# Kernel optimization log

Hardware: AMD Instinct MI355X
Metric: run time of the kernel (lower is better)

The kernel has to match this reference:

```python
import jax, jax.numpy as jnp
import numpy as np

S, B, D, T, E, H = 8, 32, 5, 30, 768, 128


def _time_lstm(Wall, ball, Uall, bU, Wd, bd, x, ts):
    # x: [N,T,E], ts: [N,T]. Faithful to torch TimeLSTM: c_tmp uses sigmoid,
    # and the returned per-step 'outputs' are the o-gates (as in the source).
    N = x.shape[0]
    h0 = jnp.zeros((N, Wd.shape[0]), x.dtype)

    def step(carry, inp):
        h, c = carry
        xt, tt = inp
        c_s1 = jnp.tanh(c @ Wd + bd)
        c_adj = c - c_s1 + c_s1 * tt[:, None]
        g = jax.nn.sigmoid(h @ Wall + ball + xt @ Uall + bU)
        f, i, o, ct = jnp.split(g, 4, axis=1)
        c2 = f * c_adj + i * ct
        h2 = o * jnp.tanh(c2)
        return (h2, c2), o

    _, outs = jax.lax.scan(step, (h0, h0), (x.swapaxes(0, 1), ts.swapaxes(0, 1)))
    return outs.swapaxes(0, 1)  # [N,T,H]


def _attn(W1, b1, W2, b2, V, bV, full, last, lens):
    # full: [N,T,H]; last: [N,H] or [N,1,H]
    s1 = last @ W1 + b1
    if s1.ndim == 2:
        s1 = s1[:, None, :]
    score = jnp.tanh(s1 + full @ W2 + b2) @ V + bV  # [N,T,1]
    if lens is not None:
        mask = jnp.arange(full.shape[1])[None, :] < lens[:, None]
        score = jnp.where(mask[..., None], score, -jnp.inf)
    w = jax.nn.softmax(score, axis=1)
    return jnp.sum(w * full, axis=1)  # [N,H]


def _lstm(Wih, bih, Whh, bhh, x):
    # standard torch LSTM gate order i,f,g,o; x: [N,D,H]
    N = x.shape[0]
    Hh = Whh.shape[0]
    h0 = jnp.zeros((N, Hh), x.dtype)

    def step(carry, xt):
        h, c = carry
        g = xt @ Wih + bih + h @ Whh + bhh
        i, f, gg, o = jnp.split(g, 4, axis=1)
        c2 = jax.nn.sigmoid(f) * c + jax.nn.sigmoid(i) * jnp.tanh(gg)
        h2 = jax.nn.sigmoid(o) * jnp.tanh(c2)
        return (h2, c2), h2

    (h, c), hs = jax.lax.scan(step, (h0, h0), x.swapaxes(0, 1))
    return hs.swapaxes(0, 1), h  # [N,D,H], [N,H]


def _per_stock(tl_Wall, tl_ball, tl_Uall, tl_bU, tl_Wd, tl_bd,
               a1_W1, a1_b1, a1_W2, a1_b2, a1_V, a1_bV,
               l2_Wih, l2_bih, l2_Whh, l2_bhh,
               a2_W1, a2_b1, a2_W2, a2_b2, a2_V, a2_bV,
               x1_W, x1_b, x2_W, x2_b, sent, lens, times):
    # sent: [B,D,T,E], lens: [B,D] int, times: [B,D,T]
    b, d, t, e = sent.shape
    x = sent.reshape(b * d, t, e)
    ts = times.reshape(b * d, t)
    ln = lens.reshape(b * d)
    outs = _time_lstm(tl_Wall, tl_ball, tl_Uall, tl_bU, tl_Wd, tl_bd, x, ts)
    idx = jnp.clip(ln - 1, 0, t - 1)
    hn = outs[jnp.arange(b * d), idx]
    hn = jnp.where((ln > 0)[:, None], hn, 0.0)
    ctx = _attn(a1_W1, a1_b1, a1_W2, a1_b2, a1_V, a1_bV, outs, hn, ln)  # [B*D,H]
    seq = ctx.reshape(b, d, -1)
    hs, hlast = _lstm(l2_Wih, l2_bih, l2_Whh, l2_bhh, seq)
    ctx2 = _attn(a2_W1, a2_b1, a2_W2, a2_b2, a2_V, a2_bV, hs, hlast[:, None, :], None)
    y = jax.nn.relu(ctx2 @ x1_W + x1_b)  # dropout is eval-mode identity
    return y @ x2_W + x2_b  # [B,64]


def setup_inputs() -> dict:
    key = jax.random.key(0)
    ks = iter(jax.random.split(key, 64))

    def p(*shape):
        return jax.random.normal(next(ks), shape, jnp.float32) * 0.05

    H4 = 4 * H
    return {
        'stock_feats': jax.random.normal(next(ks), (B, 2 * S + 1), jnp.float32),
        'sentence_feat': jax.random.normal(next(ks), (B, S, D, T, E), jnp.float32),
        'time_feats': jax.random.uniform(next(ks), (B, S, D, T), jnp.float32),
        'len_tweets': jax.random.randint(next(ks), (B, S, D), 1, T + 1),
        'tl_Wall': p(S, H, H4), 'tl_ball': p(S, H4),
        'tl_Uall': p(S, E, H4), 'tl_bU': p(S, H4),
        'tl_Wd': p(S, H, H), 'tl_bd': p(S, H),
        'a1_W1': p(S, H, H), 'a1_b1': p(S, H), 'a1_W2': p(S, H, H), 'a1_b2': p(S, H),
        'a1_V': p(S, H, 1), 'a1_bV': p(S, 1),
        'l2_Wih': p(S, H, H4), 'l2_bih': p(S, H4), 'l2_Whh': p(S, H, H4), 'l2_bhh': p(S, H4),
        'a2_W1': p(S, H, H), 'a2_b1': p(S, H), 'a2_W2': p(S, H, H), 'a2_b2': p(S, H),
        'a2_V': p(S, H, 1), 'a2_bV': p(S, 1),
        'x1_W': p(S, H, H), 'x1_b': p(S, H), 'x2_W': p(S, H, 64), 'x2_b': p(S, 64),
        'h1_W': p(2 * S + 1, 64), 'h1_b': p(64),
        'h2_W': p(64, 32), 'h2_b': p(32),
        'hc_W': p(64 * S + 32, S), 'hc_b': p(S),
    }


def reference(stock_feats, sentence_feat, time_feats, len_tweets,
              tl_Wall, tl_ball, tl_Uall, tl_bU, tl_Wd, tl_bd,
              a1_W1, a1_b1, a1_W2, a1_b2, a1_V, a1_bV,
              l2_Wih, l2_bih, l2_Whh, l2_bhh,
              a2_W1, a2_b1, a2_W2, a2_b2, a2_V, a2_bV,
              x1_W, x1_b, x2_W, x2_b,
              h1_W, h1_b, h2_W, h2_b, hc_W, hc_b):
    sent = sentence_feat.transpose(1, 0, 2, 3, 4)  # [S,B,D,T,E]
    lens = len_tweets.transpose(1, 0, 2)           # [S,B,D]
    times = time_feats.transpose(1, 0, 2, 3)       # [S,B,D,T]
    per = jax.vmap(_per_stock)(
        tl_Wall, tl_ball, tl_Uall, tl_bU, tl_Wd, tl_bd,
        a1_W1, a1_b1, a1_W2, a1_b2, a1_V, a1_bV,
        l2_Wih, l2_bih, l2_Whh, l2_bhh,
        a2_W1, a2_b1, a2_W2, a2_b2, a2_V, a2_bV,
        x1_W, x1_b, x2_W, x2_b, sent, lens, times)  # [S,B,64]
    text = per.transpose(1, 0, 2).reshape(sent.shape[1], -1)  # [B, S*64]
    xs = jax.nn.relu(stock_feats @ h1_W + h1_b) @ h2_W + h2_b  # [B,32]
    full = jnp.concatenate([xs, text], axis=1)
    return jnp.tanh(full @ hc_W + hc_b)  # [B,S]
```

## Files before the change

kernel.cpp:

```cpp
#include <hip/hip_runtime.h>
#include <cstddef>


typedef __attribute__((ext_vector_type(8))) _Float16 f16x8;
typedef __attribute__((ext_vector_type(4))) _Float16 f16x4;
typedef __attribute__((ext_vector_type(2))) _Float16 f16x2;
typedef __attribute__((ext_vector_type(4))) float f32x4;

__device__ __forceinline__ float rcp_(float x) { return __builtin_amdgcn_rcpf(x); }
__device__ __forceinline__ float sigf(float x) { return rcp_(1.0f + __expf(-x)); }
__device__ __forceinline__ float tanhf_(float x) { return 1.0f - 2.0f * rcp_(__expf(2.0f * x) + 1.0f); }

__device__ __forceinline__ void barrier_lds_only() {
  asm volatile("s_waitcnt lgkmcnt(0)" ::: "memory");
  __builtin_amdgcn_s_barrier();
  __builtin_amdgcn_sched_barrier(0);
}

__global__ __launch_bounds__(256) void k0_rowmap(const int* __restrict__ lens,
                                                 int* __restrict__ rowmap,
                                                 int* __restrict__ Ms) {
  const int s = blockIdx.x;
  const int tid = threadIdx.x;
  __shared__ int st[160];
  __shared__ int ln[160];
  if (tid < 160) {
    const int b = tid / 5, d = tid % 5;
    ln[tid] = lens[(b * 8 + s) * 5 + d];
  }
  __syncthreads();
  if (tid == 0) {
    int run = 0;
    for (int n = 0; n < 160; ++n) { st[n] = run; run += ln[n]; }
    Ms[s] = run;
  }
  __syncthreads();
  if (tid < 160) {
    const int base = st[tid], l = ln[tid];
    for (int t = 0; t < l; ++t) rowmap[s * 4800 + base + t] = tid * 30 + t;
  }
}

__global__ __launch_bounds__(256) void k0_usplit(const float* __restrict__ U,
                                                 _Float16* __restrict__ Uh) {
  const int s = blockIdx.z;
  const int k0 = blockIdx.x * 64;
  const int n0 = blockIdx.y * 64;
  const int tid = threadIdx.x;
  __shared__ _Float16 Th[64 * 66];
  const float* Us = U + (size_t)s * 768 * 512;
#pragma unroll
  for (int rep = 0; rep < 16; ++rep) {
    const int idx = rep * 256 + tid;
    const int r = idx >> 6, c = idx & 63;
    Th[r * 66 + c] = (_Float16)Us[(size_t)(k0 + r) * 512 + n0 + c];
  }
  __syncthreads();
  _Float16* uhs = Uh + (size_t)s * 512 * 768;
#pragma unroll
  for (int rep = 0; rep < 8; ++rep) {
    const int idx = rep * 256 + tid;
    const int nn = idx >> 5;
    const int kp = (idx & 31) * 2;
    const f16x2 h2 = {Th[kp * 66 + nn], Th[(kp + 1) * 66 + nn]};
    *(f16x2*)&uhs[(size_t)(n0 + nn) * 768 + k0 + kp] = h2;
  }
}

__global__ __launch_bounds__(256) void k0_wprep(const float* __restrict__ Wall,
                                                const float* __restrict__ Wd,
                                                _Float16* __restrict__ Wfh,
                                                _Float16* __restrict__ Dfh) {
  const int w = blockIdx.x, s = blockIdx.y;
  const int tid = threadIdx.x;
  const float* Ws = Wall + (size_t)s * 65536;
  _Float16* oh = Wfh + (size_t)(s * 8 + w) * 8192;
  for (int c = tid; c < 1024; c += 256) {
    const int kt = c >> 8, nt = (c >> 6) & 3, l = c & 63;
    const int n = nt * 128 + w * 16 + (l & 15);
    const int kb = kt * 32 + ((l >> 4) << 3);
    f16x8 hv;
#pragma unroll
    for (int e = 0; e < 8; ++e) hv[e] = (_Float16)Ws[(size_t)(kb + e) * 512 + n];
    *(f16x8*)&oh[c * 8] = hv;
  }
  {
    const float* Ds = Wd + (size_t)s * 16384;
    _Float16* od = Dfh + (size_t)(s * 8 + w) * 2048;
    const int c = tid;
    const int kt = c >> 6, l = c & 63;
    const int n = w * 16 + (l & 15);
    const int kb = kt * 32 + ((l >> 4) << 3);
    f16x8 hv;
#pragma unroll
    for (int e = 0; e < 8; ++e) hv[e] = (_Float16)Ds[(size_t)(kb + e) * 128 + n];
    *(f16x8*)&od[c * 8] = hv;
  }
}

__global__ __launch_bounds__(256) void k0_aprep(const float* __restrict__ W1,
                                                const float* __restrict__ W2,
                                                _Float16* __restrict__ W1f,
                                                _Float16* __restrict__ W2f) {
  const int w = blockIdx.x, s = blockIdx.y;
  const int c = threadIdx.x;
  const int kt = c >> 6, l = c & 63;
  const int n = w * 16 + (l & 15);
  const int kb = kt * 32 + ((l >> 4) << 3);
  const float* W1s = W1 + (size_t)s * 16384;
  const float* W2s = W2 + (size_t)s * 16384;
  f16x8 v1, v2;
#pragma unroll
  for (int e = 0; e < 8; ++e) {
    v1[e] = (_Float16)W1s[(size_t)(kb + e) * 128 + n];
    v2[e] = (_Float16)W2s[(size_t)(kb + e) * 128 + n];
  }
  *(f16x8*)&W1f[(size_t)(s * 8 + w) * 2048 + c * 8] = v1;
  *(f16x8*)&W2f[(size_t)(s * 8 + w) * 2048 + c * 8] = v2;
}

__global__ __launch_bounds__(256, 4) void k1_xu(const float* __restrict__ sent,
                                                const _Float16* __restrict__ Uh,
                                                const float* __restrict__ bU,
                                                const int* __restrict__ rowmap,
                                                const int* __restrict__ Ms,
                                                float* __restrict__ XU) {
  const int s = blockIdx.x;
  const int M = Ms[s];
  const int nt = blockIdx.y & 3;
  const int mt = blockIdx.y >> 2;
  if (mt * 128 >= M) return;
  const int tid = threadIdx.x;
  const int lane = tid & 63, wid = tid >> 6;
  const int wm = wid >> 1, wn = wid & 1;

  __shared__ _Float16 Al[2][128 * 32];
  __shared__ _Float16 Bh[2][128 * 32];

  const int ar1 = tid >> 2;
  const int chk = tid & 3;
  const int afk = chk * 8;
  const int fw = (ar1 ^ (ar1 >> 2)) & 3;
  const int wA1 = ar1 * 32 + ((chk ^ fw) * 8);
  const int wA2 = wA1 + 64 * 32;

  const int* rms = rowmap + s * 4800;
  const float* asrc1;
  const float* asrc2;
  {
    int i1 = mt * 128 + ar1; if (i1 > M - 1) i1 = M - 1;
    const int grow = rms[i1];
    const int nn = grow / 30, tt = grow % 30, ab = nn / 5, ad = nn % 5;
    asrc1 = sent + (size_t)((((ab * 8 + s) * 5 + ad) * 30) + tt) * 768 + afk;
  }
  {
    int i2 = mt * 128 + ar1 + 64; if (i2 > M - 1) i2 = M - 1;
    const int grow = rms[i2];
    const int nn = grow / 30, tt = grow % 30, ab = nn / 5, ad = nn % 5;
    asrc2 = sent + (size_t)((((ab * 8 + s) * 5 + ad) * 30) + tt) * 768 + afk;
  }
  const _Float16* UhS = Uh + (size_t)s * 512 * 768;
  const _Float16* bh1 = UhS + (size_t)(nt * 128 + ar1) * 768 + afk;
  const _Float16* bh2 = UhS + (size_t)(nt * 128 + ar1 + 64) * 768 + afk;

  const int q = lane >> 4;
  const int l15 = lane & 15;
  int aoff[4], boff[4];
#pragma unroll
  for (int f = 0; f < 4; ++f) {
    {
      const int row = wm * 64 + f * 16 + l15;
      const int fr = (row ^ (row >> 2)) & 3;
      aoff[f] = row * 32 + ((q ^ fr) * 8);
    }
    {
      const int row = wn * 64 + f * 16 + l15;
      const int fr = (row ^ (row >> 2)) & 3;
      boff[f] = row * 32 + ((q ^ fr) * 8);
    }
  }

  f32x4 acc[4][4];
#pragma unroll
  for (int i = 0; i < 4; ++i)
#pragma unroll
    for (int j = 0; j < 4; ++j) acc[i][j] = (f32x4){0.f, 0.f, 0.f, 0.f};

  {
    const float4 a1a = *(const float4*)(asrc1);
    const float4 a1b = *(const float4*)(asrc1 + 4);
    const float4 a2a = *(const float4*)(asrc2);
    const float4 a2b = *(const float4*)(asrc2 + 4);
    const f16x8 vh1 = *(const f16x8*)(bh1);
    const f16x8 vh2 = *(const f16x8*)(bh2);
    f16x8 h1, h2;
    h1[0]=(_Float16)a1a.x; h1[1]=(_Float16)a1a.y; h1[2]=(_Float16)a1a.z; h1[3]=(_Float16)a1a.w;
    h1[4]=(_Float16)a1b.x; h1[5]=(_Float16)a1b.y; h1[6]=(_Float16)a1b.z; h1[7]=(_Float16)a1b.w;
    h2[0]=(_Float16)a2a.x; h2[1]=(_Float16)a2a.y; h2[2]=(_Float16)a2a.z; h2[3]=(_Float16)a2a.w;
    h2[4]=(_Float16)a2b.x; h2[5]=(_Float16)a2b.y; h2[6]=(_Float16)a2b.z; h2[7]=(_Float16)a2b.w;
    *(f16x8*)&Al[0][wA1] = h1;
    *(f16x8*)&Al[0][wA2] = h2;
    *(f16x8*)&Bh[0][wA1] = vh1;
    *(f16x8*)&Bh[0][wA2] = vh2;
  }
  __syncthreads();

  int cur = 0;
  for (int ks = 0; ks < 24; ++ks) {
    const int nxt = cur ^ 1;
    const bool more = (ks < 23);
    float4 a1a, a1b, a2a, a2b;
    f16x8 vh1, vh2;
    if (more) {
      const int ko = (ks + 1) * 32;
      a1a = *(const float4*)(asrc1 + ko);
      a1b = *(const float4*)(asrc1 + ko + 4);
      a2a = *(const float4*)(asrc2 + ko);
      a2b = *(const float4*)(asrc2 + ko + 4);
      vh1 = *(const f16x8*)(bh1 + ko);
      vh2 = *(const f16x8*)(bh2 + ko);
    }
    {
      const _Float16* Ab = &Al[cur][0];
      const _Float16* Bhb = &Bh[cur][0];
      f16x8 af[4], bhf[4];
#pragma unroll
      for (int fm = 0; fm < 4; ++fm) af[fm] = *(const f16x8*)&Ab[aoff[fm]];
#pragma unroll
      for (int fn = 0; fn < 4; ++fn) bhf[fn] = *(const f16x8*)&Bhb[boff[fn]];
#pragma unroll
      for (int fm = 0; fm < 4; ++fm)
#pragma unroll
        for (int fn = 0; fn < 4; ++fn)
          acc[fm][fn] = __builtin_amdgcn_mfma_f32_16x16x32_f16(af[fm], bhf[fn], acc[fm][fn], 0, 0, 0);
    }
    if (more) {
      f16x8 h1, h2;
      h1[0]=(_Float16)a1a.x; h1[1]=(_Float16)a1a.y; h1[2]=(_Float16)a1a.z; h1[3]=(_Float16)a1a.w;
      h1[4]=(_Float16)a1b.x; h1[5]=(_Float16)a1b.y; h1[6]=(_Float16)a1b.z; h1[7]=(_Float16)a1b.w;
      h2[0]=(_Float16)a2a.x; h2[1]=(_Float16)a2a.y; h2[2]=(_Float16)a2a.z; h2[3]=(_Float16)a2a.w;
      h2[4]=(_Float16)a2b.x; h2[5]=(_Float16)a2b.y; h2[6]=(_Float16)a2b.z; h2[7]=(_Float16)a2b.w;
      *(f16x8*)&Al[nxt][wA1] = h1;
      *(f16x8*)&Al[nxt][wA2] = h2;
      *(f16x8*)&Bh[nxt][wA1] = vh1;
      *(f16x8*)&Bh[nxt][wA2] = vh2;
    }
    barrier_lds_only();
    cur = nxt;
  }

  const int lq = lane >> 4;
  const int colbase = nt * 128 + wn * 64;
  const int ibase = mt * 128 + wm * 64;
  float* XUs = XU + (size_t)s * 4800 * 512;
  int rowm[4][4];
#pragma unroll
  for (int fm = 0; fm < 4; ++fm)
#pragma unroll
    for (int r = 0; r < 4; ++r) {
      const int i = ibase + fm * 16 + lq * 4 + r;
      rowm[fm][r] = (i < M) ? rms[i] : -1;
    }
#pragma unroll
  for (int fn = 0; fn < 4; ++fn) {
    const int col = colbase + fn * 16 + l15;
    const float bias = bU[s * 512 + col];
#pragma unroll
    for (int fm = 0; fm < 4; ++fm)
#pragma unroll
      for (int r = 0; r < 4; ++r) {
        const int row = rowm[fm][r];
        if (row >= 0) XUs[(size_t)row * 512 + col] = acc[fm][fn][r] + bias;
      }
  }
}

__global__ __launch_bounds__(512, 2) void k2_tlstm(const _Float16* __restrict__ Wfh,
                                                   const _Float16* __restrict__ Dfh,
                                                   const float* __restrict__ ball,
                                                   const float* __restrict__ bd,
                                                   const float* __restrict__ XU,
                                                   const float* __restrict__ times,
                                                   const int* __restrict__ lens,
                                                   float* __restrict__ outs,
                                                   float* __restrict__ hn) {
  const int s = blockIdx.x;
  const int mg = blockIdx.y;
  const int tid = threadIdx.x;
  const int w = tid >> 6, l = tid & 63;

  __shared__ _Float16 hhb[2][2048];
  __shared__ _Float16 chb[2][2048];
  __shared__ float xut[2][16 * 516];
  __shared__ float tsh[16 * 32];
  __shared__ int lensh[16];

  if (tid < 16) {
    const int n = mg * 16 + tid;
    lensh[tid] = lens[((n / 5) * 8 + s) * 5 + (n % 5)];
  }
  if (tid < 480) {
    const int r = tid / 30, c = tid % 30;
    const int n = mg * 16 + r;
    tsh[r * 32 + c] = times[(((n / 5) * 8 + s) * 5 + (n % 5)) * 30 + c];
  }

  f16x8 Bh[16], Dh[4];
  {
    const _Float16* wb = Wfh + (size_t)(s * 8 + w) * 8192 + l * 8;
    const _Float16* db = Dfh + (size_t)(s * 8 + w) * 2048 + l * 8;
#pragma unroll
    for (int c = 0; c < 16; ++c) Bh[c] = *(const f16x8*)&wb[c * 512];
#pragma unroll
    for (int c = 0; c < 4; ++c) Dh[c] = *(const f16x8*)&db[c * 512];
  }

  const int hd = w * 16 + (l & 15);
  const int rq0 = (l >> 4) * 4;
  const int lp0 = rq0 | (((hd >> 3) & 3) << 4);
  const int eoff0 = ((hd >> 5) * 64 + lp0) * 8 + (hd & 7);

#pragma unroll
  for (int q = 0; q < 4; ++q) {
    hhb[0][eoff0 + q * 8] = (_Float16)0.f;
    chb[0][eoff0 + q * 8] = (_Float16)0.f;
  }

  int n_q[4];
#pragma unroll
  for (int q = 0; q < 4; ++q) n_q[q] = mg * 16 + rq0 + q;
  float blr[4];
#pragma unroll
  for (int g = 0; g < 4; ++g) blr[g] = ball[s * 512 + g * 128 + hd];
  const float bdj = bd[s * 128 + hd];

  const int sr = tid >> 5;
  const int sc = tid & 31;
  const float* xsrc = XU + (size_t)(s * 160 + mg * 16 + sr) * 30 * 512 + sc * 4;
  const int xdst = sr * 516 + sc * 4;

  __syncthreads();

  int len_q[4];
  int maxlen = 0;
#pragma unroll
  for (int i = 0; i < 16; ++i) maxlen = max(maxlen, lensh[i]);
#pragma unroll
  for (int q = 0; q < 4; ++q) len_q[q] = lensh[rq0 + q];

  float creg[4] = {0.f, 0.f, 0.f, 0.f};
  float hreg[4] = {0.f, 0.f, 0.f, 0.f};
  float oprev[4] = {0.f, 0.f, 0.f, 0.f};

  {
    float4 v0 = *(const float4*)(xsrc);
    float4 v1 = *(const float4*)(xsrc + 128);
    float4 v2 = *(const float4*)(xsrc + 256);
    float4 v3 = *(const float4*)(xsrc + 384);
    *(float4*)&xut[0][xdst]       = v0;
    *(float4*)&xut[0][xdst + 128] = v1;
    *(float4*)&xut[0][xdst + 256] = v2;
    *(float4*)&xut[0][xdst + 384] = v3;
  }
  __syncthreads();

  for (int t = 0; t < maxlen; ++t) {
    const int p = t & 1;

    if (t > 0) {
      const int tp = t - 1;
#pragma unroll
      for (int q = 0; q < 4; ++q) {
        if (tp < len_q[q]) {
          outs[((size_t)(s * 160 + n_q[q]) * 30 + tp) * 128 + hd] = oprev[q];
          if (tp == len_q[q] - 1) hn[(size_t)(s * 160 + n_q[q]) * 128 + hd] = oprev[q];
        }
      }
    }

    float4 pv0, pv1, pv2, pv3;
    const bool more = (t + 1 < maxlen);
    if (more) {
      const float* xp = xsrc + (size_t)(t + 1) * 512;
      pv0 = *(const float4*)(xp);
      pv1 = *(const float4*)(xp + 128);
      pv2 = *(const float4*)(xp + 256);
      pv3 = *(const float4*)(xp + 384);
    }

    f32x4 amA[4], amB[4], dm;
#pragma unroll
    for (int g = 0; g < 4; ++g) {
      amA[g] = (f32x4){0.f, 0.f, 0.f, 0.f};
      amB[g] = (f32x4){0.f, 0.f, 0.f, 0.f};
    }
    dm = (f32x4){0.f, 0.f, 0.f, 0.f};
#pragma unroll
    for (int kt = 0; kt < 2; ++kt) {
      const f16x8 ah0 = *(const f16x8*)&hhb[p][(kt * 64 + l) * 8];
      const f16x8 ah1 = *(const f16x8*)&hhb[p][((kt + 2) * 64 + l) * 8];
      const f16x8 cf0 = *(const f16x8*)&chb[p][(kt * 64 + l) * 8];
      const f16x8 cf1 = *(const f16x8*)&chb[p][((kt + 2) * 64 + l) * 8];
#pragma unroll
      for (int g = 0; g < 4; ++g) {
        amA[g] = __builtin_amdgcn_mfma_f32_16x16x32_f16(ah0, Bh[kt * 4 + g], amA[g], 0, 0, 0);
        amB[g] = __builtin_amdgcn_mfma_f32_16x16x32_f16(ah1, Bh[(kt + 2) * 4 + g], amB[g], 0, 0, 0);
      }
      dm = __builtin_amdgcn_mfma_f32_16x16x32_f16(cf0, Dh[kt], dm, 0, 0, 0);
      dm = __builtin_amdgcn_mfma_f32_16x16x32_f16(cf1, Dh[kt + 2], dm, 0, 0, 0);
    }

#pragma unroll
    for (int q = 0; q < 4; ++q) {
      if (t < len_q[q]) {
        const float* xr = &xut[p][(rq0 + q) * 516 + hd];
        const float tt = tsh[(rq0 + q) * 32 + t];
        const float cs1 = tanhf_(dm[q] + bdj);
        const float f  = sigf(amA[0][q] + amB[0][q] + xr[0]   + blr[0]);
        const float ii = sigf(amA[1][q] + amB[1][q] + xr[128] + blr[1]);
        const float o  = sigf(amA[2][q] + amB[2][q] + xr[256] + blr[2]);
        const float ct = sigf(amA[3][q] + amB[3][q] + xr[384] + blr[3]);
        const float c2 = f * (creg[q] + cs1 * (tt - 1.f)) + ii * ct;
        creg[q] = c2;
        hreg[q] = o * tanhf_(c2);
        oprev[q] = o;
      }
      hhb[p ^ 1][eoff0 + q * 8] = (_Float16)hreg[q];
      chb[p ^ 1][eoff0 + q * 8] = (_Float16)creg[q];
    }

    if (more) {
      *(float4*)&xut[p ^ 1][xdst]       = pv0;
      *(float4*)&xut[p ^ 1][xdst + 128] = pv1;
      *(float4*)&xut[p ^ 1][xdst + 256] = pv2;
      *(float4*)&xut[p ^ 1][xdst + 384] = pv3;
    }
    barrier_lds_only();
  }

  {
    const int tp = maxlen - 1;
#pragma unroll
    for (int q = 0; q < 4; ++q) {
      if (tp >= 0 && tp < len_q[q]) {
        outs[((size_t)(s * 160 + n_q[q]) * 30 + tp) * 128 + hd] = oprev[q];
        if (tp == len_q[q] - 1) hn[(size_t)(s * 160 + n_q[q]) * 128 + hd] = oprev[q];
      }
    }
  }
}

__global__ __launch_bounds__(512, 2) void k3_attn1(const _Float16* __restrict__ W1f,
                                                   const _Float16* __restrict__ W2f,
                                                   const float* __restrict__ b1,
                                                   const float* __restrict__ b2,
                                                   const float* __restrict__ V,
                                                   const float* __restrict__ outs,
                                                   const float* __restrict__ hn,
                                                   const int* __restrict__ lens,
                                                   float* __restrict__ ctx) {
  const int s = blockIdx.x;
  const int sg = blockIdx.y;
  const int tid = threadIdx.x;
  const int w = tid >> 6, l = tid & 63;
  const int nbase = s * 160 + sg * 8;

  __shared__ _Float16 osh[32768];
  __shared__ float u[16][132];
  __shared__ float red[8][8][32];
  __shared__ float score[8][32];
  __shared__ int lensh[8];

  if (tid < 8) {
    const int n = sg * 8 + tid;
    lensh[tid] = lens[((n / 5) * 8 + s) * 5 + (n % 5)];
  }

#pragma unroll
  for (int i = 0; i < 8; ++i) {
    const int c = tid + i * 512;
    const int nl = c >> 9;
    const int th = (c >> 8) & 1;
    const int kt = (c >> 6) & 3;
    const int lp = c & 63;
    const int t15 = lp & 15;
    const int kb = kt * 32 + (lp >> 4) * 8;
    const int t = th * 16 + t15;
    f16x8 v;
    if (t < 30) {
      const float* src = outs + ((size_t)(nbase + nl) * 30 + t) * 128 + kb;
      const float4 a = *(const float4*)(src);
      const float4 b = *(const float4*)(src + 4);
      v[0]=(_Float16)a.x; v[1]=(_Float16)a.y; v[2]=(_Float16)a.z; v[3]=(_Float16)a.w;
      v[4]=(_Float16)b.x; v[5]=(_Float16)b.y; v[6]=(_Float16)b.z; v[7]=(_Float16)b.w;
    } else {
      v = (f16x8){(_Float16)0.f,(_Float16)0.f,(_Float16)0.f,(_Float16)0.f,
                  (_Float16)0.f,(_Float16)0.f,(_Float16)0.f,(_Float16)0.f};
    }
    *(f16x8*)&osh[c * 8] = v;
  }

  f16x8 W1r[4], W2r[4];
  {
    const _Float16* w1b = W1f + (size_t)(s * 8 + w) * 2048 + l * 8;
    const _Float16* w2b = W2f + (size_t)(s * 8 + w) * 2048 + l * 8;
#pragma unroll
    for (int kt = 0; kt < 4; ++kt) {
      W1r[kt] = *(const f16x8*)&w1b[kt * 512];
      W2r[kt] = *(const f16x8*)&w2b[kt * 512];
    }
  }

  const int hd = w * 16 + (l & 15);
  const float Vhd = V[s * 128 + hd];
  const float b12 = b1[s * 128 + hd] + b2[s * 128 + hd];
  const int kc = (l >> 4) << 3;

  {
    const int rsrc = min(l & 15, 7);
    f32x4 dm = (f32x4){0.f, 0.f, 0.f, 0.f};
#pragma unroll
    for (int kt = 0; kt < 4; ++kt) {
      const float* hp = hn + (size_t)(nbase + rsrc) * 128 + kt * 32 + kc;
      const float4 a = *(const float4*)(hp);
      const float4 b = *(const float4*)(hp + 4);
      f16x8 ah;
      ah[0]=(_Float16)a.x; ah[1]=(_Float16)a.y; ah[2]=(_Float16)a.z; ah[3]=(_Float16)a.w;
      ah[4]=(_Float16)b.x; ah[5]=(_Float16)b.y; ah[6]=(_Float16)b.z; ah[7]=(_Float16)b.w;
      dm = __builtin_amdgcn_mfma_f32_16x16x32_f16(ah, W1r[kt], dm, 0, 0, 0);
    }
#pragma unroll
    for (int q = 0; q < 4; ++q) u[(l >> 4) * 4 + q][hd] = dm[q] + b12;
  }
  __syncthreads();

#pragma unroll
  for (int m = 0; m < 16; ++m) {
    const int nl = m >> 1, th = m & 1;
    const int cbase = ((nl * 2 + th) * 4) * 64;
    f32x4 acc = (f32x4){0.f, 0.f, 0.f, 0.f};
#pragma unroll
    for (int kt = 0; kt < 4; ++kt) {
      const f16x8 ah = *(const f16x8*)&osh[(cbase + kt * 64 + l) * 8];
      acc = __builtin_amdgcn_mfma_f32_16x16x32_f16(ah, W2r[kt], acc, 0, 0, 0);
    }
    const float uv = u[nl][hd];
#pragma unroll
    for (int q = 0; q < 4; ++q) {
      float p = tanhf_(acc[q] + uv) * Vhd;
      p += __shfl_xor(p, 1);
      p += __shfl_xor(p, 2);
      p += __shfl_xor(p, 4);
      p += __shfl_xor(p, 8);
      const int t = th * 16 + (l >> 4) * 4 + q;
      if ((l & 15) == 0 && t < 30) red[w][nl][t] = p;
    }
  }
  __syncthreads();

  if (tid < 256) {
    const int nl = tid >> 5, t = tid & 31;
    if (t < 30) {
      float sc = 0.f;
#pragma unroll
      for (int ww = 0; ww < 8; ++ww) sc += red[ww][nl][t];
      score[nl][t] = sc;
    }
  }
  __syncthreads();

  {
    const int nl = tid >> 6, jg = tid & 63;
    const int len = lensh[nl];
    float mx = -1e30f;
    for (int t = 0; t < len; ++t) mx = fmaxf(mx, score[nl][t]);
    const float* ob = outs + (size_t)(nbase + nl) * 30 * 128 + jg * 2;
    float sum = 0.f;
    float cx0 = 0.f, cx1 = 0.f;
    for (int t = 0; t < len; ++t) {
      const float e = __expf(score[nl][t] - mx);
      sum += e;
      const float2 o2 = *(const float2*)(ob + (size_t)t * 128);
      cx0 += e * o2.x; cx1 += e * o2.y;
    }
    const float r = rcp_(sum);
    float2 res = {cx0 * r, cx1 * r};
    *(float2*)&ctx[(size_t)(nbase + nl) * 128 + jg * 2] = res;
  }
}

__global__ __launch_bounds__(512, 2) void k4_lstm2(const float* __restrict__ Wih,
                                                   const float* __restrict__ bih,
                                                   const float* __restrict__ Whh,
                                                   const float* __restrict__ bhh,
                                                   const float* __restrict__ ctx,
                                                   float* __restrict__ hsout,
                                                   float* __restrict__ hlast) {
  const int s = blockIdx.y, b = blockIdx.x;
  const int gj = threadIdx.x;
  __shared__ float xs[5][128];
  __shared__ float hsm[128];
  __shared__ float gsh[512];

  for (int idx = gj; idx < 640; idx += 512)
    (&xs[0][0])[idx] = ctx[(size_t)(s * 160 + b * 5) * 128 + idx];
  if (gj < 128) hsm[gj] = 0.f;
  __syncthreads();

  const float* Wis = Wih + (size_t)s * 65536;
  const float* Whs = Whh + (size_t)s * 65536;
  const float bias = bih[s * 512 + gj] + bhh[s * 512 + gj];
  float xw[5] = {bias, bias, bias, bias, bias};
  float whh[128];
#pragma unroll
  for (int k = 0; k < 128; ++k) {
    const float wi = Wis[k * 512 + gj];
    whh[k] = Whs[k * 512 + gj];
#pragma unroll
    for (int dd = 0; dd < 5; ++dd) xw[dd] += xs[dd][k] * wi;
  }

  float c = 0.f;
  for (int dd = 0; dd < 5; ++dd) {
    float g = xw[dd];
#pragma unroll
    for (int k = 0; k < 128; ++k) g += hsm[k] * whh[k];
    gsh[gj] = g;
    __syncthreads();
    if (gj < 128) {
      const int j = gj;
      const float c2 = sigf(gsh[128 + j]) * c + sigf(gsh[j]) * tanhf_(gsh[256 + j]);
      const float h2 = sigf(gsh[384 + j]) * tanhf_(c2);
      c = c2;
      hsm[j] = h2;
      hsout[((size_t)(s * 32 + b) * 5 + dd) * 128 + j] = h2;
      if (dd == 4) hlast[(size_t)(s * 32 + b) * 128 + j] = h2;
    }
    __syncthreads();
  }
}

__global__ __launch_bounds__(128) void k5_attn2(const float* __restrict__ W1,
                                                const float* __restrict__ b1,
                                                const float* __restrict__ W2,
                                                const float* __restrict__ b2,
                                                const float* __restrict__ V,
                                                const float* __restrict__ bV,
                                                const float* __restrict__ x1W,
                                                const float* __restrict__ x1b,
                                                const float* __restrict__ x2W,
                                                const float* __restrict__ x2b,
                                                const float* __restrict__ hs,
                                                const float* __restrict__ hlast,
                                                float* __restrict__ y) {
  const int s = blockIdx.y, b = blockIdx.x, j = threadIdx.x;
  __shared__ float hl[128], hsm[5][128], t1[128], cs2[128], sc[5], red[2];
  hl[j] = hlast[(size_t)(s * 32 + b) * 128 + j];
  const float* hsrc = hs + (size_t)(s * 32 + b) * 640;
  for (int idx = j; idx < 640; idx += 128) (&hsm[0][0])[idx] = hsrc[idx];
  __syncthreads();

  const float* W1s = W1 + (size_t)s * 16384;
  const float* W2s = W2 + (size_t)s * 16384;
  float u = b1[s * 128 + j] + b2[s * 128 + j];
  for (int k = 0; k < 128; ++k) u += hl[k] * W1s[k * 128 + j];
  const float Vj = V[s * 128 + j];
  const int lane = j & 63, wid = j >> 6;

  for (int d = 0; d < 5; ++d) {
    float a = u;
    for (int k = 0; k < 128; ++k) a += hsm[d][k] * W2s[k * 128 + j];
    float p = tanhf_(a) * Vj;
#pragma unroll
    for (int off = 32; off; off >>= 1) p += __shfl_down(p, off);
    if (lane == 0) red[wid] = p;
    __syncthreads();
    if (j == 0) sc[d] = red[0] + red[1] + bV[s];
    __syncthreads();
  }

  float m = -1e30f;
  for (int d = 0; d < 5; ++d) m = fmaxf(m, sc[d]);
  float sum = 0.f;
  for (int d = 0; d < 5; ++d) sum += __expf(sc[d] - m);
  float cx = 0.f;
  for (int d = 0; d < 5; ++d) cx += __expf(sc[d] - m) * hsm[d][j];
  cs2[j] = cx / sum;
  __syncthreads();

  float a = x1b[s * 128 + j];
  for (int k = 0; k < 128; ++k) a += cs2[k] * x1W[(size_t)s * 16384 + k * 128 + j];
  t1[j] = fmaxf(a, 0.f);
  __syncthreads();

  if (j < 64) {
    float yy = x2b[s * 64 + j];
    for (int k = 0; k < 128; ++k) yy += t1[k] * x2W[(size_t)(s * 128 + k) * 64 + j];
    y[(size_t)(s * 32 + b) * 64 + j] = yy;
  }
}

__global__ __launch_bounds__(256) void k6_final(const float* __restrict__ stock,
                                                const float* __restrict__ h1W,
                                                const float* __restrict__ h1b,
                                                const float* __restrict__ h2W,
                                                const float* __restrict__ h2b,
                                                const float* __restrict__ hcW,
                                                const float* __restrict__ hcb,
                                                const float* __restrict__ yws,
                                                float* __restrict__ out) {
  const int tid = threadIdx.x;
  __shared__ float sf[32 * 17];
  __shared__ float hid[32 * 64];
  __shared__ float xs[32 * 32];
  for (int idx = tid; idx < 544; idx += 256) sf[idx] = stock[idx];
  __syncthreads();
  for (int idx = tid; idx < 2048; idx += 256) {
    const int b = idx >> 6, k = idx & 63;
    float a = h1b[k];
    for (int q = 0; q < 17; ++q) a += sf[b * 17 + q] * h1W[q * 64 + k];
    hid[idx] = fmaxf(a, 0.f);
  }
  __syncthreads();
  for (int idx = tid; idx < 1024; idx += 256) {
    const int b = idx >> 5, mm = idx & 31;
    float a = h2b[mm];
    for (int k = 0; k < 64; ++k) a += hid[b * 64 + k] * h2W[k * 32 + mm];
    xs[idx] = a;
  }
  __syncthreads();
  {
    const int b = tid >> 3, o = tid & 7;
    float a = hcb[o];
    for (int c = 0; c < 32; ++c) a += xs[b * 32 + c] * hcW[c * 8 + o];
    for (int c = 32; c < 544; ++c) {
      const int ss = (c - 32) >> 6, k = (c - 32) & 63;
      a += yws[((size_t)ss * 32 + b) * 64 + k] * hcW[c * 8 + o];
    }
    out[tid] = tanhf_(a);
  }
}

extern "C" void kernel_launch(void* const* d_in, const int* in_sizes, int n_in,
                              void* d_out, int out_size, void* d_ws, size_t ws_size,
                              hipStream_t stream) {
  (void)in_sizes; (void)n_in; (void)out_size; (void)ws_size;
  const float* stock = (const float*)d_in[0];
  const float* sent  = (const float*)d_in[1];
  const float* times = (const float*)d_in[2];
  const int*   lens  = (const int*)d_in[3];
  const float* tlWall = (const float*)d_in[4];
  const float* tlball = (const float*)d_in[5];
  const float* tlUall = (const float*)d_in[6];
  const float* tlbU   = (const float*)d_in[7];
  const float* tlWd   = (const float*)d_in[8];
  const float* tlbd   = (const float*)d_in[9];
  const float* a1W1 = (const float*)d_in[10];
  const float* a1b1 = (const float*)d_in[11];
  const float* a1W2 = (const float*)d_in[12];
  const float* a1b2 = (const float*)d_in[13];
  const float* a1V  = (const float*)d_in[14];
  const float* a1bV = (const float*)d_in[15];
  const float* l2Wih = (const float*)d_in[16];
  const float* l2bih = (const float*)d_in[17];
  const float* l2Whh = (const float*)d_in[18];
  const float* l2bhh = (const float*)d_in[19];
  const float* a2W1 = (const float*)d_in[20];
  const float* a2b1 = (const float*)d_in[21];
  const float* a2W2 = (const float*)d_in[22];
  const float* a2b2 = (const float*)d_in[23];
  const float* a2V  = (const float*)d_in[24];
  const float* a2bV = (const float*)d_in[25];
  const float* x1W  = (const float*)d_in[26];
  const float* x1b  = (const float*)d_in[27];
  const float* x2W  = (const float*)d_in[28];
  const float* x2b  = (const float*)d_in[29];
  const float* h1W  = (const float*)d_in[30];
  const float* h1b  = (const float*)d_in[31];
  const float* h2W  = (const float*)d_in[32];
  const float* h2b  = (const float*)d_in[33];
  const float* hcW  = (const float*)d_in[34];
  const float* hcb  = (const float*)d_in[35];

  float* ws = (float*)d_ws;
  float* XU    = ws;
  float* outs  = XU + 19660800;
  float* hnb   = outs + 4915200;
  float* ctx   = hnb + 163840;
  float* hsb   = ctx + 163840;
  float* hlast = hsb + 163840;
  float* yb    = hlast + 32768;
  _Float16* Uhw = (_Float16*)(yb + 16384);
  _Float16* Wfh = Uhw + 8 * 512 * 768;
  _Float16* Dfh = Wfh + 8 * 8 * 8192;
  _Float16* W1f = Dfh + 8 * 8 * 2048;
  _Float16* W2f = W1f + 8 * 8 * 2048;
  int* rowmap = (int*)(W2f + 8 * 8 * 2048);
  int* Msd    = rowmap + 8 * 4800;

  k0_rowmap<<<8, 256, 0, stream>>>(lens, rowmap, Msd);
  k0_usplit<<<dim3(12, 8, 8), 256, 0, stream>>>(tlUall, Uhw);
  k0_wprep<<<dim3(8, 8), 256, 0, stream>>>(tlWall, tlWd, Wfh, Dfh);
  k0_aprep<<<dim3(8, 8), 256, 0, stream>>>(a1W1, a1W2, W1f, W2f);
  k1_xu<<<dim3(8, 152), 256, 0, stream>>>(sent, Uhw, tlbU, rowmap, Msd, XU);
  k2_tlstm<<<dim3(8, 10), 512, 0, stream>>>(Wfh, Dfh, tlball, tlbd, XU, times, lens, outs, hnb);
  k3_attn1<<<dim3(8, 20), 512, 0, stream>>>(W1f, W2f, a1b1, a1b2, a1V, outs, hnb, lens, ctx);
  k4_lstm2<<<dim3(32, 8), 512, 0, stream>>>(l2Wih, l2bih, l2Whh, l2bhh, ctx, hsb, hlast);
  k5_attn2<<<dim3(32, 8), 128, 0, stream>>>(a2W1, a2b1, a2W2, a2b2, a2V, a2bV, x1W, x1b, x2W, x2b, hsb, hlast, yb);
  k6_final<<<1, 256, 0, stream>>>(stock, h1W, h1b, h2W, h2b, hcW, hcb, yb, (float*)d_out);
}
```

Before: 215.9 us.

## Fuse second LSTM and attention/MLP head into one kernel with split-K

Merges the word-level LSTM kernel with the second attention and the x1/x2 MLP kernel, so hidden states stay in shared memory and are not written to and reread from global memory. One kernel launch is removed. The attention and MLP matvecs now use all 512 threads, with the K dimension split four or eight ways and reduced through shared memory, where before they ran on 128 threads. The softmax bias bV is dropped because it is shift-invariant. This adds extra barriers and shared-memory use inside the fused kernel.

```diff
diff --git a/kernel.cpp b/kernel.cpp
--- a/kernel.cpp
+++ b/kernel.cpp
@@ -589,33 +589,49 @@
   }
 }
 
-__global__ __launch_bounds__(512, 2) void k4_lstm2(const float* __restrict__ Wih,
-                                                   const float* __restrict__ bih,
-                                                   const float* __restrict__ Whh,
-                                                   const float* __restrict__ bhh,
-                                                   const float* __restrict__ ctx,
-                                                   float* __restrict__ hsout,
-                                                   float* __restrict__ hlast) {
+__global__ __launch_bounds__(512, 2) void k45_fused(const float* __restrict__ Wih,
+                                                    const float* __restrict__ bih,
+                                                    const float* __restrict__ Whh,
+                                                    const float* __restrict__ bhh,
+                                                    const float* __restrict__ aW1,
+                                                    const float* __restrict__ ab1,
+                                                    const float* __restrict__ aW2,
+                                                    const float* __restrict__ ab2,
+                                                    const float* __restrict__ aV,
+                                                    const float* __restrict__ x1W,
+                                                    const float* __restrict__ x1b,
+                                                    const float* __restrict__ x2W,
+                                                    const float* __restrict__ x2b,
+                                                    const float* __restrict__ ctx,
+                                                    float* __restrict__ y) {
   const int s = blockIdx.y, b = blockIdx.x;
-  const int gj = threadIdx.x;
+  const int tid = threadIdx.x;
   __shared__ float xs[5][128];
-  __shared__ float hsm[128];
+  __shared__ float hsm[5][128];
+  __shared__ float hcur[128];
   __shared__ float gsh[512];
-
-  for (int idx = gj; idx < 640; idx += 512)
+  __shared__ float red[4][128];
+  __shared__ float wred[2];
+  __shared__ float sc[5];
+  __shared__ float u_sh[128];
+  __shared__ float cs2[128];
+  __shared__ float t1[128];
+  __shared__ float red2[8][64];
+
+  for (int idx = tid; idx < 640; idx += 512)
     (&xs[0][0])[idx] = ctx[(size_t)(s * 160 + b * 5) * 128 + idx];
-  if (gj < 128) hsm[gj] = 0.f;
+  if (tid < 128) hcur[tid] = 0.f;
   __syncthreads();
 
   const float* Wis = Wih + (size_t)s * 65536;
   const float* Whs = Whh + (size_t)s * 65536;
-  const float bias = bih[s * 512 + gj] + bhh[s * 512 + gj];
+  const float bias = bih[s * 512 + tid] + bhh[s * 512 + tid];
   float xw[5] = {bias, bias, bias, bias, bias};
   float whh[128];
 #pragma unroll
   for (int k = 0; k < 128; ++k) {
-    const float wi = Wis[k * 512 + gj];
-    whh[k] = Whs[k * 512 + gj];
+    const float wi = Wis[k * 512 + tid];
+    whh[k] = Whs[k * 512 + tid];
 #pragma unroll
     for (int dd = 0; dd < 5; ++dd) xw[dd] += xs[dd][k] * wi;
   }
@@ -624,79 +640,92 @@
   for (int dd = 0; dd < 5; ++dd) {
     float g = xw[dd];
 #pragma unroll
-    for (int k = 0; k < 128; ++k) g += hsm[k] * whh[k];
-    gsh[gj] = g;
+    for (int k = 0; k < 128; ++k) g += hcur[k] * whh[k];
+    gsh[tid] = g;
     __syncthreads();
-    if (gj < 128) {
-      const int j = gj;
+    if (tid < 128) {
+      const int j = tid;
       const float c2 = sigf(gsh[128 + j]) * c + sigf(gsh[j]) * tanhf_(gsh[256 + j]);
       const float h2 = sigf(gsh[384 + j]) * tanhf_(c2);
       c = c2;
-      hsm[j] = h2;
-      hsout[((size_t)(s * 32 + b) * 5 + dd) * 128 + j] = h2;
-      if (dd == 4) hlast[(size_t)(s * 32 + b) * 128 + j] = h2;
+      hcur[j] = h2;
+      hsm[dd][j] = h2;
     }
     __syncthreads();
   }
-}
-
-__global__ __launch_bounds__(128) void k5_attn2(const float* __restrict__ W1,
-                                                const float* __restrict__ b1,
-                                                const float* __restrict__ W2,
-                                                const float* __restrict__ b2,
-                                                const float* __restrict__ V,
-                                                const float* __restrict__ bV,
-                                                const float* __restrict__ x1W,
-                                                const float* __restrict__ x1b,
-                                                const float* __restrict__ x2W,
-                                                const float* __restrict__ x2b,
-                                                const float* __restrict__ hs,
-                                                const float* __restrict__ hlast,
-                                                float* __restrict__ y) {
-  const int s = blockIdx.y, b = blockIdx.x, j = threadIdx.x;
-  __shared__ float hl[128], hsm[5][128], t1[128], cs2[128], sc[5], red[2];
-  hl[j] = hlast[(size_t)(s * 32 + b) * 128 + j];
-  const float* hsrc = hs + (size_t)(s * 32 + b) * 640;
-  for (int idx = j; idx < 640; idx += 128) (&hsm[0][0])[idx] = hsrc[idx];
-  __syncthreads();
-
-  const float* W1s = W1 + (size_t)s * 16384;
-  const float* W2s = W2 + (size_t)s * 16384;
-  float u = b1[s * 128 + j] + b2[s * 128 + j];
-  for (int k = 0; k < 128; ++k) u += hl[k] * W1s[k * 128 + j];
-  const float Vj = V[s * 128 + j];
-  const int lane = j & 63, wid = j >> 6;
+
+  const int q = tid >> 7, j = tid & 127;
+  const float* W1s = aW1 + (size_t)s * 16384;
+  const float* W2s = aW2 + (size_t)s * 16384;
+
+  {
+    float part = 0.f;
+#pragma unroll
+    for (int k = 0; k < 32; ++k) part += hsm[4][q * 32 + k] * W1s[(q * 32 + k) * 128 + j];
+    red[q][j] = part;
+  }
+  __syncthreads();
+  if (tid < 128)
+    u_sh[j] = red[0][j] + red[1][j] + red[2][j] + red[3][j] +
+              ab1[s * 128 + j] + ab2[s * 128 + j];
+  __syncthreads();
 
   for (int d = 0; d < 5; ++d) {
-    float a = u;
-    for (int k = 0; k < 128; ++k) a += hsm[d][k] * W2s[k * 128 + j];
-    float p = tanhf_(a) * Vj;
-#pragma unroll
-    for (int off = 32; off; off >>= 1) p += __shfl_down(p, off);
-    if (lane == 0) red[wid] = p;
+    float part = 0.f;
+#pragma unroll
+    for (int k = 0; k < 32; ++k) part += hsm[d][q * 32 + k] * W2s[(q * 32 + k) * 128 + j];
+    red[q][j] = part;
     __syncthreads();
-    if (j == 0) sc[d] = red[0] + red[1] + bV[s];
+    if (tid < 128) {
+      float a = u_sh[j] + red[0][j] + red[1][j] + red[2][j] + red[3][j];
+      float pv = tanhf_(a) * aV[s * 128 + j];
+#pragma unroll
+      for (int off = 32; off; off >>= 1) pv += __shfl_down(pv, off);
+      if ((tid & 63) == 0) wred[tid >> 6] = pv;
+    }
     __syncthreads();
-  }
-
-  float m = -1e30f;
-  for (int d = 0; d < 5; ++d) m = fmaxf(m, sc[d]);
-  float sum = 0.f;
-  for (int d = 0; d < 5; ++d) sum += __expf(sc[d] - m);
-  float cx = 0.f;
-  for (int d = 0; d < 5; ++d) cx += __expf(sc[d] - m) * hsm[d][j];
-  cs2[j] = cx / sum;
-  __syncthreads();
-
-  float a = x1b[s * 128 + j];
-  for (int k = 0; k < 128; ++k) a += cs2[k] * x1W[(size_t)s * 16384 + k * 128 + j];
-  t1[j] = fmaxf(a, 0.f);
-  __syncthreads();
-
-  if (j < 64) {
-    float yy = x2b[s * 64 + j];
-    for (int k = 0; k < 128; ++k) yy += t1[k] * x2W[(size_t)(s * 128 + k) * 64 + j];
-    y[(size_t)(s * 32 + b) * 64 + j] = yy;
+    if (tid == 0) sc[d] = wred[0] + wred[1];
+    __syncthreads();
+  }
+
+  if (tid < 128) {
+    float m = sc[0];
+#pragma unroll
+    for (int d = 1; d < 5; ++d) m = fmaxf(m, sc[d]);
+    float e[5], sum = 0.f;
+#pragma unroll
+    for (int d = 0; d < 5; ++d) { e[d] = __expf(sc[d] - m); sum += e[d]; }
+    float cx = 0.f;
+#pragma unroll
+    for (int d = 0; d < 5; ++d) cx += e[d] * hsm[d][j];
+    cs2[j] = cx * rcp_(sum);
+  }
+  __syncthreads();
+
+  {
+    float part = 0.f;
+#pragma unroll
+    for (int k = 0; k < 32; ++k) part += cs2[q * 32 + k] * x1W[(size_t)s * 16384 + (q * 32 + k) * 128 + j];
+    red[q][j] = part;
+  }
+  __syncthreads();
+  if (tid < 128)
+    t1[j] = fmaxf(red[0][j] + red[1][j] + red[2][j] + red[3][j] + x1b[s * 128 + j], 0.f);
+  __syncthreads();
+
+  {
+    const int q2 = tid >> 6, j2 = tid & 63;
+    float part = 0.f;
+#pragma unroll
+    for (int k = 0; k < 16; ++k) part += t1[q2 * 16 + k] * x2W[(size_t)s * 8192 + (q2 * 16 + k) * 64 + j2];
+    red2[q2][j2] = part;
+  }
+  __syncthreads();
+  if (tid < 64) {
+    float yy = x2b[s * 64 + tid];
+#pragma unroll
+    for (int g = 0; g < 8; ++g) yy += red2[g][tid];
+    y[(size_t)(s * 32 + b) * 64 + tid] = yy;
   }
 }
 
@@ -781,15 +810,14 @@
   const float* h2b  = (const float*)d_in[33];
   const float* hcW  = (const float*)d_in[34];
   const float* hcb  = (const float*)d_in[35];
+  (void)a1bV; (void)a2bV;
 
   float* ws = (float*)d_ws;
   float* XU    = ws;
   float* outs  = XU + 19660800;
   float* hnb   = outs + 4915200;
   float* ctx   = hnb + 163840;
-  float* hsb   = ctx + 163840;
-  float* hlast = hsb + 163840;
-  float* yb    = hlast + 32768;
+  float* yb    = ctx + 163840;
   _Float16* Uhw = (_Float16*)(yb + 16384);
   _Float16* Wfh = Uhw + 8 * 512 * 768;
   _Float16* Dfh = Wfh + 8 * 8 * 8192;
@@ -805,7 +833,8 @@
   k1_xu<<<dim3(8, 152), 256, 0, stream>>>(sent, Uhw, tlbU, rowmap, Msd, XU);
   k2_tlstm<<<dim3(8, 10), 512, 0, stream>>>(Wfh, Dfh, tlball, tlbd, XU, times, lens, outs, hnb);
   k3_attn1<<<dim3(8, 20), 512, 0, stream>>>(W1f, W2f, a1b1, a1b2, a1V, outs, hnb, lens, ctx);
-  k4_lstm2<<<dim3(32, 8), 512, 0, stream>>>(l2Wih, l2bih, l2Whh, l2bhh, ctx, hsb, hlast);
-  k5_attn2<<<dim3(32, 8), 128, 0, stream>>>(a2W1, a2b1, a2W2, a2b2, a2V, a2bV, x1W, x1b, x2W, x2b, hsb, hlast, yb);
+  k45_fused<<<dim3(32, 8), 512, 0, stream>>>(l2Wih, l2bih, l2Whh, l2bhh,
+                                             a2W1, a2b1, a2W2, a2b2, a2V,
+                                             x1W, x1b, x2W, x2b, ctx, yb);
   k6_final<<<1, 256, 0, stream>>>(stock, h1W, h1b, h2W, h2b, hcW, hcb, yb, (float*)d_out);
 }
```

Result: faster. 201.3 us, median of 2 (-6.8%).
